# Kernel optimization log

Measured on AMD Instinct MI355X. Metric: run time of the kernel, lower is better.

## Reference

```python
import jax, jax.numpy as jnp
from jax import lax
import numpy as np

EPS = 1e-5
N_BITS = 2   # sign-random-projection hash bits
U = 0.999    # ALSH filter rescale constant (from module args)


def _conv(x, w, b):
    # 3x3, stride 1, pad 1, NCHW/OIHW
    y = lax.conv_general_dilated(x, w, (1, 1), ((1, 1), (1, 1)),
                                 dimension_numbers=('NCHW', 'OIHW', 'NCHW'))
    return y + b[None, :, None, None]


def _bn2d(x, g, b):
    m = x.mean((0, 2, 3), keepdims=True)
    v = x.var((0, 2, 3), keepdims=True)
    return (x - m) * lax.rsqrt(v + EPS) * g[None, :, None, None] + b[None, :, None, None]


def _bn1d(x, g, b):
    m = x.mean(0)
    v = x.var(0)
    return (x - m) * lax.rsqrt(v + EPS) * g + b


def _pool(x):
    return lax.reduce_window(x, -jnp.inf, lax.max, (1, 1, 2, 2), (1, 1, 2, 2), 'VALID')


def _alsh_mask(x, w6, hash_a):
    # ALSH-MIPS filter selection with SignRandomProjection.
    C_out = w6.shape[0]
    wf = w6.reshape(C_out, -1)                       # (256, 2304)
    norms = jnp.linalg.norm(wf, axis=1)
    wf_s = wf * (U / jnp.max(norms))                 # rescale so max norm = U
    ns = jnp.linalg.norm(wf_s, axis=1)
    # P = append_sub_norm_powers (m=2): [w, ||w||^2, ||w||^4]
    P = jnp.concatenate([wf_s, (ns ** 2)[:, None], (ns ** 4)[:, None]], axis=1)
    # Query: mean input patch (per-channel mean tiled over 3x3 taps), normalized
    q = x.mean((0, 2, 3))                            # (256,)
    qv = jnp.tile(q, 9)
    qv = qv / (jnp.linalg.norm(qv) + 1e-12)
    Q = jnp.concatenate([qv, jnp.zeros((2,), x.dtype)])  # append_zeros (m=2)
    bits_f = (P @ hash_a.T) > 0                      # (256, N_BITS)
    bits_q = (Q @ hash_a.T) > 0                      # (N_BITS,)
    pw = 2 ** jnp.arange(N_BITS)
    code_f = (bits_f * pw).sum(1)
    code_q = (bits_q * pw).sum()
    return lax.stop_gradient((code_f == code_q).astype(x.dtype))  # (256,)


def setup_inputs() -> dict:
    key = jax.random.key(0)
    ks = jax.random.split(key, 12)
    B = 256
    d = {}
    d['x'] = jax.random.normal(ks[0], (B, 3, 32, 32), jnp.float32)
    conv_shapes = [(64, 3), (64, 64), (128, 64), (128, 128), (256, 128), (256, 256)]
    for i, (co, ci) in enumerate(conv_shapes, start=1):
        d[f'w{i}'] = jax.random.normal(ks[i], (co, ci, 3, 3), jnp.float32) * 0.05
        d[f'b{i}'] = jnp.zeros((co,), jnp.float32)
        d[f'g{i}'] = jnp.ones((co,), jnp.float32)
        d[f'be{i}'] = jnp.zeros((co,), jnp.float32)
    d['hash_a'] = jax.random.normal(ks[7], (N_BITS, 256 * 9 + 2), jnp.float32)
    d['fc7_w'] = jax.random.normal(ks[8], (512, 4096), jnp.float32) * 0.02
    d['fc7_b'] = jnp.zeros((512,), jnp.float32)
    d['g7'] = jnp.ones((512,), jnp.float32)
    d['be7'] = jnp.zeros((512,), jnp.float32)
    d['fc8_w'] = jax.random.normal(ks[9], (512, 512), jnp.float32) * 0.02
    d['fc8_b'] = jnp.zeros((512,), jnp.float32)
    d['g8'] = jnp.ones((512,), jnp.float32)
    d['be8'] = jnp.zeros((512,), jnp.float32)
    d['fc9_w'] = jax.random.normal(ks[10], (10, 512), jnp.float32) * 0.02
    d['fc9_b'] = jnp.zeros((10,), jnp.float32)
    return d


def reference(x, w1, b1, g1, be1, w2, b2, g2, be2, w3, b3, g3, be3,
              w4, b4, g4, be4, w5, b5, g5, be5, w6, b6, g6, be6, hash_a,
              fc7_w, fc7_b, g7, be7, fc8_w, fc8_b, g8, be8, fc9_w, fc9_b):
    B = x.shape[0]
    x = jax.nn.relu(_bn2d(_conv(x, w1, b1), g1, be1))
    x = jax.nn.relu(_bn2d(_conv(x, w2, b2), g2, be2))
    x = _pool(x)                                   # (B,64,16,16)
    x = jax.nn.relu(_bn2d(_conv(x, w3, b3), g3, be3))
    x = jax.nn.relu(_bn2d(_conv(x, w4, b4), g4, be4))
    x = _pool(x)                                   # (B,128,8,8)
    x = jax.nn.relu(_bn2d(_conv(x, w5, b5), g5, be5))  # (B,256,8,8)
    # ALSH conv6: compute only hash-matched filters, zero-fill the rest.
    mask = _alsh_mask(x, w6, hash_a)               # (256,)
    x = _conv(x, w6, b6) * mask[None, :, None, None]   # subset conv + zero_fill_missing
    x = jax.nn.relu(_bn2d(x, g6, be6))
    x = _pool(x)                                   # (B,256,4,4)
    x = x.reshape(B, -1)                           # (B,4096)
    x = jax.nn.relu(_bn1d(x @ fc7_w.T + fc7_b, g7, be7))
    x = jax.nn.relu(_bn1d(x @ fc8_w.T + fc8_b, g8, be8))
    return x @ fc9_w.T + fc9_b                     # (B,10)
```

## Files before the change

### kernel.cpp

```cpp
#include <hip/hip_runtime.h>

typedef unsigned short u16;
typedef unsigned int u32;
typedef __attribute__((ext_vector_type(8))) _Float16 f16x8;
typedef __attribute__((ext_vector_type(4))) float f32x4;

#define U_CONST 0.999f

constexpr size_t OFFB_STATS = 0;
constexpr size_t OFFB_WSTAT = 14336;
constexpr size_t OFFB_MASK  = 18432;
constexpr size_t OFFB_FCIN  = 32768;
constexpr size_t OFFB_W7T   = 2129920;
constexpr size_t OFFB_W8T   = 6324224;
constexpr size_t OFFB_P7    = 6848512;
constexpr size_t OFFB_P8    = 15237120;
constexpr size_t OFFB_A7    = 19431424;
constexpr size_t OFFB_A8    = 19693568;
constexpr size_t OFFB_WT2   = 20971520;
constexpr size_t OFFB_WT3   = 21045248;
constexpr size_t OFFB_WT4   = 21192704;
constexpr size_t OFFB_WT5   = 21487616;
constexpr size_t OFFB_WT6   = 22077440;
constexpr size_t OFFB_SLAB1 = 25165824;
constexpr size_t OFFB_SLAB2 = 60817408;
constexpr size_t OFFB_PART  = OFFB_P7;
constexpr size_t OFFB_QPART = OFFB_P8;

__device__ __forceinline__ u16 f2h(float f) {
  _Float16 h = (_Float16)f;
  return __builtin_bit_cast(u16, h);
}
__device__ __forceinline__ float h2f(u16 u) {
  return (float)__builtin_bit_cast(_Float16, u);
}
__device__ __forceinline__ void gload16(const void* g, void* l) {
  __builtin_amdgcn_global_load_lds(
      (const __attribute__((address_space(1))) unsigned int*)g,
      (__attribute__((address_space(3))) unsigned int*)l, 16, 0, 0);
}

__global__ __launch_bounds__(256) void k_xform_x(const float* __restrict__ x,
                                                 float* __restrict__ xt) {
  int idx = blockIdx.x * 256 + threadIdx.x;
  if (idx >= 256 * 3 * 1024) return;
  int c = idx % 3;
  int t = idx / 3;
  int s = t % 1024;
  int b = t / 1024;
  xt[idx] = x[(b * 3 + c) * 1024 + s];
}

__global__ __launch_bounds__(256) void k_xform_w(const float* __restrict__ w,
                                                 u16* __restrict__ wt, int CO,
                                                 int CI) {
  int total = CO * CI * 9;
  for (int idx = blockIdx.x * 256 + threadIdx.x; idx < total;
       idx += gridDim.x * 256) {
    int ci = idx % CI;
    int t = idx / CI;
    int co = t % CO;
    int tap = t / CO;
    wt[idx] = f2h(w[(co * CI + ci) * 9 + tap]);
  }
}

__global__ __launch_bounds__(256) void k_cvt_h(const float* __restrict__ w,
                                               u16* __restrict__ o, int n) {
  for (int i = blockIdx.x * 256 + threadIdx.x; i < n; i += gridDim.x * 256)
    o[i] = f2h(w[i]);
}

__global__ __launch_bounds__(256) void k_conv1(const float* __restrict__ xt,
                                               const float* __restrict__ w1,
                                               const float* __restrict__ b1,
                                               u16* __restrict__ y,
                                               float* __restrict__ part) {
  __shared__ float Ins[4 * 34 * 3];
  __shared__ float Ws[27 * 64];
  __shared__ float sred[64 * 16 * 2];
  int tid = threadIdx.x;
  int m0 = blockIdx.x * 64;
  int b = m0 >> 10;
  int y0 = (m0 & 1023) >> 5;

  for (int i = tid; i < 27 * 64; i += 256) {
    int co = i & 63;
    int t = i >> 6;
    int ci = t % 3;
    int tap = t / 3;
    Ws[i] = w1[co * 27 + ci * 9 + tap];
  }
  for (int i = tid; i < 4 * 34 * 3; i += 256) {
    int ci = i % 3;
    int t = i / 3;
    int xx = t % 34;
    int yy = t / 34;
    int gy = y0 - 1 + yy;
    int gx = xx - 1;
    float v = 0.f;
    if ((unsigned)gy < 32u && (unsigned)gx < 32u)
      v = xt[((b * 32 + gy) * 32 + gx) * 3 + ci];
    Ins[i] = v;
  }
  __syncthreads();

  int tr = tid >> 4, tc = tid & 15;
  float acc[4][4] = {};
#pragma unroll
  for (int tap = 0; tap < 9; tap++) {
    int dy = tap / 3, dx = tap % 3;
#pragma unroll
    for (int ci = 0; ci < 3; ci++) {
      float4 wv = *(const float4*)&Ws[(tap * 3 + ci) * 64 + tc * 4];
#pragma unroll
      for (int i = 0; i < 4; i++) {
        int r = tr * 4 + i;
        int yy = (r >> 5) + dy;
        int xx = (r & 31) + dx;
        float a = Ins[(yy * 34 + xx) * 3 + ci];
        acc[i][0] += a * wv.x;
        acc[i][1] += a * wv.y;
        acc[i][2] += a * wv.z;
        acc[i][3] += a * wv.w;
      }
    }
  }
  float4 bb = *(const float4*)&b1[tc * 4];
  float cs[4] = {}, cq[4] = {};
#pragma unroll
  for (int i = 0; i < 4; i++) {
    size_t r = (size_t)(m0 + tr * 4 + i);
    float v0 = acc[i][0] + bb.x, v1 = acc[i][1] + bb.y;
    float v2 = acc[i][2] + bb.z, v3 = acc[i][3] + bb.w;
    cs[0] += v0; cq[0] += v0 * v0;
    cs[1] += v1; cq[1] += v1 * v1;
    cs[2] += v2; cq[2] += v2 * v2;
    cs[3] += v3; cq[3] += v3 * v3;
    u32 lo = (u32)f2h(v0) | ((u32)f2h(v1) << 16);
    u32 hi = (u32)f2h(v2) | ((u32)f2h(v3) << 16);
    *(uint2*)&y[r * 64 + tc * 4] = make_uint2(lo, hi);
  }
#pragma unroll
  for (int q = 0; q < 4; q++) {
    sred[((tc * 4 + q) * 16 + tr) * 2] = cs[q];
    sred[((tc * 4 + q) * 16 + tr) * 2 + 1] = cq[q];
  }
  __syncthreads();
  if (tid < 64) {
    float s = 0.f, q = 0.f;
#pragma unroll
    for (int t = 0; t < 16; t++) {
      s += sred[(tid * 16 + t) * 2];
      q += sred[(tid * 16 + t) * 2 + 1];
    }
    part[(size_t)tid * gridDim.x + blockIdx.x] = s;
    part[(size_t)(64 + tid) * gridDim.x + blockIdx.x] = q;
  }
}

template <int CIN, int COUT, int H, int W, bool MASKED>
__global__ __launch_bounds__(256) void k_cmfma(
    const u16* __restrict__ inp, const u16* __restrict__ wt,
    const float* __restrict__ bias, const float* __restrict__ mask,
    u16* __restrict__ out, float* __restrict__ part) {
  constexpr int HW = H * W;
  __shared__ __align__(16) u16 ldsA[128 * 64];
  __shared__ __align__(16) u16 ldsB[64 * 64];
  const int tid = threadIdx.x;
  const int wave = tid >> 6, lane = tid & 63;
  const int m0 = blockIdx.x * 128;
  const int n0 = blockIdx.y * 64;
  const int ss = (lane & 7) ^ (lane >> 3);
  const u16* aptr[4];
#pragma unroll
  for (int q = 0; q < 4; q++) {
    int m = m0 + wave * 32 + q * 8 + (lane >> 3);
    int b = m / HW, rem = m % HW;
    int yy = rem / W, xx = rem % W;
    aptr[q] = inp +
              ((size_t)((b * (H + 2) + yy + 1) * (W + 2)) + xx + 1) * CIN +
              ss * 8;
  }
  const u16* bptr[2];
#pragma unroll
  for (int q = 0; q < 2; q++) {
    int rb = wave * 16 + q * 8 + (lane >> 3);
    bptr[q] = wt + (size_t)(n0 + rb) * CIN + ss * 8;
  }
  u16* lA = ldsA + wave * 32 * 64;
  u16* lB = ldsB + wave * 16 * 64;
  const int arow0 = wave * 32 + (lane & 15);
  const int nrow = lane & 15;
  const int t0 = lane >> 4, x7 = lane & 7;
  f32x4 acc[2][4] = {};

#pragma unroll 1
  for (int tap = 0; tap < 9; tap++) {
    const int aoff = (tap / 3 - 1) * ((W + 2) * CIN) + (tap % 3 - 1) * CIN;
    const size_t woff = (size_t)tap * COUT * CIN;
#pragma unroll 1
    for (int c0 = 0; c0 < CIN; c0 += 64) {
      __syncthreads();
#pragma unroll
      for (int q = 0; q < 4; q++) gload16(aptr[q] + aoff + c0, lA + q * 512);
#pragma unroll
      for (int q = 0; q < 2; q++) gload16(bptr[q] + woff + c0, lB + q * 512);
      __syncthreads();
#pragma unroll
      for (int h = 0; h < 2; h++) {
        const int sl = (((h << 2) + t0) ^ x7) * 8;
        f16x8 af[2], bf[4];
#pragma unroll
        for (int i = 0; i < 2; i++)
          af[i] = *(const f16x8*)&ldsA[(arow0 + i * 16) * 64 + sl];
#pragma unroll
        for (int j = 0; j < 4; j++)
          bf[j] = *(const f16x8*)&ldsB[(nrow + j * 16) * 64 + sl];
#pragma unroll
        for (int i = 0; i < 2; i++)
#pragma unroll
          for (int j = 0; j < 4; j++)
            acc[i][j] = __builtin_amdgcn_mfma_f32_16x16x32_f16(
                af[i], bf[j], acc[i][j], 0, 0, 0);
      }
    }
  }
  float bn[4], mk[4];
#pragma unroll
  for (int j = 0; j < 4; j++) {
    int n = n0 + j * 16 + nrow;
    bn[j] = bias[n];
    mk[j] = MASKED ? mask[n] : 1.f;
  }
  float ps[4] = {}, pq[4] = {};
#pragma unroll
  for (int i = 0; i < 2; i++)
#pragma unroll
    for (int r = 0; r < 4; r++) {
      int m = m0 + wave * 32 + i * 16 + (lane >> 4) * 4 + r;
#pragma unroll
      for (int j = 0; j < 4; j++) {
        float v = acc[i][j][r] + bn[j];
        if (MASKED) v *= mk[j];
        out[(size_t)m * COUT + n0 + j * 16 + nrow] = f2h(v);
        ps[j] += v;
        pq[j] += v * v;
      }
    }
#pragma unroll
  for (int j = 0; j < 4; j++) {
    ps[j] += __shfl_xor(ps[j], 16);
    pq[j] += __shfl_xor(pq[j], 16);
    ps[j] += __shfl_xor(ps[j], 32);
    pq[j] += __shfl_xor(pq[j], 32);
  }
  __syncthreads();
  float* red = (float*)ldsA;
  if (lane < 16) {
#pragma unroll
    for (int j = 0; j < 4; j++) {
      red[(wave * 64 + j * 16 + lane) * 2] = ps[j];
      red[(wave * 64 + j * 16 + lane) * 2 + 1] = pq[j];
    }
  }
  __syncthreads();
  if (tid < 64) {
    float s = 0.f, q = 0.f;
#pragma unroll
    for (int w = 0; w < 4; w++) {
      s += red[(w * 64 + tid) * 2];
      q += red[(w * 64 + tid) * 2 + 1];
    }
    part[(size_t)(n0 + tid) * gridDim.x + blockIdx.x] = s;
    part[(size_t)(COUT + n0 + tid) * gridDim.x + blockIdx.x] = q;
  }
}

__global__ __launch_bounds__(256) void k_redstat(const float* __restrict__ part,
                                                 float* __restrict__ stats,
                                                 int NB, int C) {
  int c = blockIdx.x;
  const float* ps = part + (size_t)c * NB;
  const float* pq = part + (size_t)(C + c) * NB;
  int tid = threadIdx.x;
  float s = 0.f, q = 0.f;
  for (int t = tid; t < NB; t += 256) {
    s += ps[t];
    q += pq[t];
  }
#pragma unroll
  for (int off = 32; off > 0; off >>= 1) {
    s += __shfl_xor(s, off);
    q += __shfl_xor(q, off);
  }
  __shared__ float r2[4][2];
  int wave = tid >> 6, lane = tid & 63;
  if (lane == 0) {
    r2[wave][0] = s;
    r2[wave][1] = q;
  }
  __syncthreads();
  if (tid == 0) {
    stats[c * 2] = r2[0][0] + r2[1][0] + r2[2][0] + r2[3][0];
    stats[c * 2 + 1] = r2[0][1] + r2[1][1] + r2[2][1] + r2[3][1];
  }
}

__global__ __launch_bounds__(256) void k_qred(const float* __restrict__ qpart,
                                              float* __restrict__ qstat,
                                              int NB) {
  int c = blockIdx.x;
  const float* ps = qpart + (size_t)c * NB;
  int tid = threadIdx.x;
  float s = 0.f;
  for (int t = tid; t < NB; t += 256) s += ps[t];
#pragma unroll
  for (int off = 32; off > 0; off >>= 1) s += __shfl_xor(s, off);
  __shared__ float r2[4];
  int wave = tid >> 6, lane = tid & 63;
  if (lane == 0) r2[wave] = s;
  __syncthreads();
  if (tid == 0) qstat[c] = r2[0] + r2[1] + r2[2] + r2[3];
}

template <int C, int H, int W, bool QSUM>
__global__ __launch_bounds__(256) void k_bnrelu_pad(
    const u16* __restrict__ y, float invN, const float* __restrict__ st,
    const float* __restrict__ g, const float* __restrict__ be,
    u16* __restrict__ outp, float* __restrict__ qpart) {
  constexpr int CH8 = C / 8, HP = H + 2, WP = W + 2;
  __shared__ float sA[C], sB[C];
  __shared__ float qred[QSUM ? 4 : 1][32][8];
  int tid = threadIdx.x;
  if (tid < C) {
    float mu = st[tid * 2] * invN;
    float var = st[tid * 2 + 1] * invN - mu * mu;
    float sc = g[tid] * rsqrtf(var + 1e-5f);
    sA[tid] = sc;
    sB[tid] = be[tid] - mu * sc;
  }
  __syncthreads();
  float qs[8] = {};
  const size_t T = (size_t)256 * HP * WP * CH8;
  for (size_t i = (size_t)blockIdx.x * 256 + tid; i < T;
       i += (size_t)gridDim.x * 256) {
    int slot = (int)(i % CH8);
    size_t t = i / CH8;
    int xx = (int)(t % WP);
    t /= WP;
    int yy = (int)(t % HP);
    int b = (int)(t / HP);
    uint4 o;
    if (yy == 0 || yy == HP - 1 || xx == 0 || xx == WP - 1) {
      o = make_uint4(0u, 0u, 0u, 0u);
    } else {
      uint4 v =
          ((const uint4*)y)[(((size_t)(b * H + yy - 1) * W) + xx - 1) * CH8 +
                            slot];
      u32 pv[4] = {v.x, v.y, v.z, v.w};
      u32 po[4];
      int c0 = slot * 8;
#pragma unroll
      for (int k = 0; k < 4; k++) {
        int c = c0 + 2 * k;
        float lo = fmaxf(h2f((u16)(pv[k] & 0xffffu)) * sA[c] + sB[c], 0.f);
        float hi =
            fmaxf(h2f((u16)(pv[k] >> 16)) * sA[c + 1] + sB[c + 1], 0.f);
        if (QSUM) {
          qs[2 * k] += lo;
          qs[2 * k + 1] += hi;
        }
        po[k] = (u32)f2h(lo) | ((u32)f2h(hi) << 16);
      }
      o = make_uint4(po[0], po[1], po[2], po[3]);
    }
    ((uint4*)outp)[i] = o;
  }
  if (QSUM) {
    int wave = tid >> 6, lane = tid & 63;
#pragma unroll
    for (int j = 0; j < 8; j++) qs[j] += __shfl_xor(qs[j], 32);
    if (lane < 32) {
#pragma unroll
      for (int j = 0; j < 8; j++) qred[wave][lane][j] = qs[j];
    }
    __syncthreads();
    int slot = tid >> 3, jj = tid & 7;
    float s = qred[0][slot][jj] + qred[1][slot][jj] + qred[2][slot][jj] +
              qred[3][slot][jj];
    qpart[(size_t)(slot * 8 + jj) * gridDim.x + blockIdx.x] = s;
  }
}

template <int C, int H, int W, bool NCHW>
__global__ __launch_bounds__(256) void k_bnpool(
    const u16* __restrict__ y, float invN, const float* __restrict__ st,
    const float* __restrict__ g, const float* __restrict__ be,
    void* __restrict__ outv) {
  constexpr int CH8 = C / 8, HO = H / 2, WO = W / 2;
  constexpr int HP = NCHW ? HO : HO + 2, WP = NCHW ? WO : WO + 2;
  __shared__ float sA[C], sB[C];
  int tid = threadIdx.x;
  if (tid < C) {
    float mu = st[tid * 2] * invN;
    float var = st[tid * 2 + 1] * invN - mu * mu;
    float sc = g[tid] * rsqrtf(var + 1e-5f);
    sA[tid] = sc;
    sB[tid] = be[tid] - mu * sc;
  }
  __syncthreads();
  const size_t T = (size_t)256 * HP * WP * CH8;
  for (size_t i = (size_t)blockIdx.x * 256 + tid; i < T;
       i += (size_t)gridDim.x * 256) {
    int slot = (int)(i % CH8);
    size_t t = i / CH8;
    int xx = (int)(t % WP);
    t /= WP;
    int yy = (int)(t % HP);
    int b = (int)(t / HP);
    int px, py;
    bool border = false;
    if (NCHW) {
      px = xx;
      py = yy;
    } else {
      px = xx - 1;
      py = yy - 1;
      border = (yy == 0 || yy == HP - 1 || xx == 0 || xx == WP - 1);
    }
    if (border) {
      ((uint4*)outv)[i] = make_uint4(0u, 0u, 0u, 0u);
      continue;
    }
    const uint4* yp = (const uint4*)y;
    size_t i00 = (((size_t)(b * H + 2 * py) * W) + 2 * px) * CH8 + slot;
    uint4 v00 = yp[i00], v01 = yp[i00 + CH8];
    uint4 v10 = yp[i00 + (size_t)W * CH8], v11 = yp[i00 + (size_t)W * CH8 + CH8];
    u32 p00[4] = {v00.x, v00.y, v00.z, v00.w};
    u32 p01[4] = {v01.x, v01.y, v01.z, v01.w};
    u32 p10[4] = {v10.x, v10.y, v10.z, v10.w};
    u32 p11[4] = {v11.x, v11.y, v11.z, v11.w};
    int c0 = slot * 8;
    float r[8];
#pragma unroll
    for (int k = 0; k < 4; k++) {
      int c = c0 + 2 * k;
      float a_ = sA[c], b_ = sB[c], a2 = sA[c + 1], b2 = sB[c + 1];
      float l0 = fmaxf(h2f((u16)(p00[k] & 0xffffu)) * a_ + b_, 0.f);
      float l1 = fmaxf(h2f((u16)(p01[k] & 0xffffu)) * a_ + b_, 0.f);
      float l2 = fmaxf(h2f((u16)(p10[k] & 0xffffu)) * a_ + b_, 0.f);
      float l3 = fmaxf(h2f((u16)(p11[k] & 0xffffu)) * a_ + b_, 0.f);
      float h0 = fmaxf(h2f((u16)(p00[k] >> 16)) * a2 + b2, 0.f);
      float h1 = fmaxf(h2f((u16)(p01[k] >> 16)) * a2 + b2, 0.f);
      float h2 = fmaxf(h2f((u16)(p10[k] >> 16)) * a2 + b2, 0.f);
      float h3 = fmaxf(h2f((u16)(p11[k] >> 16)) * a2 + b2, 0.f);
      r[2 * k] = fmaxf(fmaxf(l0, l1), fmaxf(l2, l3));
      r[2 * k + 1] = fmaxf(fmaxf(h0, h1), fmaxf(h2, h3));
    }
    if (NCHW) {
      u16* of = (u16*)outv;
#pragma unroll
      for (int j = 0; j < 8; j++)
        of[((size_t)(b * C + c0 + j) * HO + py) * WO + px] = f2h(r[j]);
    } else {
      u32 po[4];
#pragma unroll
      for (int k = 0; k < 4; k++)
        po[k] = (u32)f2h(r[2 * k]) | ((u32)f2h(r[2 * k + 1]) << 16);
      ((uint4*)outv)[i] = make_uint4(po[0], po[1], po[2], po[3]);
    }
  }
}

template <int K, int KSPLIT>
__global__ __launch_bounds__(256) void k_fcmfma(const u16* __restrict__ a,
                                                const u16* __restrict__ w,
                                                float* __restrict__ p) {
  constexpr int KCH = K / KSPLIT;
  __shared__ __align__(16) u16 ldsA[128 * 64];
  __shared__ __align__(16) u16 ldsB[64 * 64];
  const int tid = threadIdx.x;
  const int wave = tid >> 6, lane = tid & 63;
  const int m0 = blockIdx.x * 128;
  const int n0 = blockIdx.y * 64;
  const int ks = blockIdx.z;
  const int ss = (lane & 7) ^ (lane >> 3);
  const u16* aptr[4];
#pragma unroll
  for (int q = 0; q < 4; q++)
    aptr[q] = a + (size_t)(m0 + wave * 32 + q * 8 + (lane >> 3)) * K + ss * 8;
  const u16* bptr[2];
#pragma unroll
  for (int q = 0; q < 2; q++)
    bptr[q] = w + (size_t)(n0 + wave * 16 + q * 8 + (lane >> 3)) * K + ss * 8;
  u16* lA = ldsA + wave * 32 * 64;
  u16* lB = ldsB + wave * 16 * 64;
  const int arow0 = wave * 32 + (lane & 15);
  const int nrow = lane & 15;
  const int t0 = lane >> 4, x7 = lane & 7;
  f32x4 acc[2][4] = {};

#pragma unroll 1
  for (int kc = ks * KCH; kc < ks * KCH + KCH; kc += 64) {
    __syncthreads();
#pragma unroll
    for (int q = 0; q < 4; q++) gload16(aptr[q] + kc, lA + q * 512);
#pragma unroll
    for (int q = 0; q < 2; q++) gload16(bptr[q] + kc, lB + q * 512);
    __syncthreads();
#pragma unroll
    for (int h = 0; h < 2; h++) {
      const int sl = (((h << 2) + t0) ^ x7) * 8;
      f16x8 af[2], bf[4];
#pragma unroll
      for (int i = 0; i < 2; i++)
        af[i] = *(const f16x8*)&ldsA[(arow0 + i * 16) * 64 + sl];
#pragma unroll
      for (int j = 0; j < 4; j++)
        bf[j] = *(const f16x8*)&ldsB[(nrow + j * 16) * 64 + sl];
#pragma unroll
      for (int i = 0; i < 2; i++)
#pragma unroll
        for (int j = 0; j < 4; j++)
          acc[i][j] = __builtin_amdgcn_mfma_f32_16x16x32_f16(
              af[i], bf[j], acc[i][j], 0, 0, 0);
    }
  }
  float* po = p + (size_t)ks * (256 * 512);
#pragma unroll
  for (int i = 0; i < 2; i++)
#pragma unroll
    for (int r = 0; r < 4; r++) {
      int m = m0 + wave * 32 + i * 16 + (lane >> 4) * 4 + r;
#pragma unroll
      for (int j = 0; j < 4; j++)
        po[(size_t)m * 512 + n0 + j * 16 + nrow] = acc[i][j][r];
    }
}

template <int NS>
__global__ __launch_bounds__(256) void k_bn1dfuse(const float* __restrict__ p,
                                                  const float* __restrict__ g,
                                                  const float* __restrict__ be,
                                                  u16* __restrict__ outp) {
  int wave = threadIdx.x >> 6, lane = threadIdx.x & 63;
  int c = blockIdx.x * 4 + wave;
  float v[4] = {};
#pragma unroll 1
  for (int s = 0; s < NS; s++) {
    const float* ps = p + (size_t)s * (256 * 512);
#pragma unroll
    for (int r = 0; r < 4; r++) v[r] += ps[(size_t)(lane + r * 64) * 512 + c];
  }
  float s1 = v[0] + v[1] + v[2] + v[3];
  float s2 = v[0] * v[0] + v[1] * v[1] + v[2] * v[2] + v[3] * v[3];
#pragma unroll
  for (int off = 32; off > 0; off >>= 1) {
    s1 += __shfl_xor(s1, off);
    s2 += __shfl_xor(s2, off);
  }
  float mu = s1 * (1.f / 256.f);
  float var = s2 * (1.f / 256.f) - mu * mu;
  float sc = g[c] * rsqrtf(var + 1e-5f);
  float sh = be[c] - mu * sc;
#pragma unroll
  for (int r = 0; r < 4; r++) {
    float y = fmaxf(v[r] * sc + sh, 0.f);
    outp[(size_t)(lane + r * 64) * 512 + c] = f2h(y);
  }
}

__global__ __launch_bounds__(256) void k_fc9(const u16* __restrict__ a,
                                             const float* __restrict__ w,
                                             const float* __restrict__ bias,
                                             float* __restrict__ out) {
  int b = blockIdx.x, tid = threadIdx.x;
  int o = tid & 15, ch = tid >> 4;
  float s = 0.f;
  if (o < 10) {
    const u16* ap = a + (size_t)b * 512 + ch * 32;
    const float* wp = w + (size_t)o * 512 + ch * 32;
#pragma unroll
    for (int k = 0; k < 32; k++) s += h2f(ap[k]) * wp[k];
  }
  __shared__ float red[16][17];
  red[ch][o] = s;
  __syncthreads();
  if (tid < 10) {
    float t = bias[tid];
#pragma unroll
    for (int c2 = 0; c2 < 16; c2++) t += red[c2][tid];
    out[b * 10 + tid] = t;
  }
}

__global__ __launch_bounds__(256) void k_w6stats(const float* __restrict__ w6,
                                                 const float* __restrict__ ha,
                                                 float* __restrict__ wstats) {
  int f = blockIdx.x, tid = threadIdx.x;
  const float* wp = w6 + (size_t)f * 2304;
  float ss = 0.f, d0 = 0.f, d1 = 0.f;
#pragma unroll
  for (int k = 0; k < 9; k++) {
    float v = wp[k * 256 + tid];
    ss += v * v;
    d0 += v * ha[k * 256 + tid];
    d1 += v * ha[2306 + k * 256 + tid];
  }
  for (int off = 32; off > 0; off >>= 1) {
    ss += __shfl_down(ss, off);
    d0 += __shfl_down(d0, off);
    d1 += __shfl_down(d1, off);
  }
  __shared__ float r[4][3];
  int wv = tid >> 6, ln = tid & 63;
  if (ln == 0) {
    r[wv][0] = ss;
    r[wv][1] = d0;
    r[wv][2] = d1;
  }
  __syncthreads();
  if (tid == 0) {
    float a0 = 0.f, a1 = 0.f, a2 = 0.f;
    for (int i = 0; i < 4; i++) {
      a0 += r[i][0];
      a1 += r[i][1];
      a2 += r[i][2];
    }
    wstats[f * 4 + 0] = a0;
    wstats[f * 4 + 1] = a1;
    wstats[f * 4 + 2] = a2;
  }
}

__global__ __launch_bounds__(256) void k_mask(const float* __restrict__ wstats,
                                              const float* __restrict__ qstats,
                                              const float* __restrict__ ha,
                                              float invN,
                                              float* __restrict__ mask) {
  int tid = threadIdx.x;
  __shared__ float red[256];
  float n2 = wstats[tid * 4];
  red[tid] = n2;
  __syncthreads();
  for (int off = 128; off > 0; off >>= 1) {
    if (tid < off) red[tid] = fmaxf(red[tid], red[tid + off]);
    __syncthreads();
  }
  float maxn2 = red[0];
  float qm = qstats[tid] * invN;
  float h0 = 0.f, h1 = 0.f;
#pragma unroll
  for (int k = 0; k < 9; k++) {
    h0 += ha[k * 256 + tid];
    h1 += ha[2306 + k * 256 + tid];
  }
  __shared__ float r0[256], r1[256];
  r0[tid] = qm * h0;
  r1[tid] = qm * h1;
  __syncthreads();
  for (int off = 128; off > 0; off >>= 1) {
    if (tid < off) {
      r0[tid] += r0[tid + off];
      r1[tid] += r1[tid + off];
    }
    __syncthreads();
  }
  float qd0 = r0[0], qd1 = r1[0];
  float s = U_CONST / sqrtf(maxn2);
  float ns2 = s * s * wstats[tid * 4];
  float v0 = s * wstats[tid * 4 + 1] + ns2 * ha[2304] + ns2 * ns2 * ha[2305];
  float v1 = s * wstats[tid * 4 + 2] + ns2 * ha[2306 + 2304] +
             ns2 * ns2 * ha[2306 + 2305];
  bool bf0 = v0 > 0.f, bf1 = v1 > 0.f;
  bool bq0 = qd0 > 0.f, bq1 = qd1 > 0.f;
  mask[tid] = (bf0 == bq0 && bf1 == bq1) ? 1.f : 0.f;
}

extern "C" void kernel_launch(void* const* d_in, const int* in_sizes, int n_in,
                              void* d_out, int out_size, void* d_ws,
                              size_t ws_size, hipStream_t stream) {
  (void)in_sizes; (void)n_in; (void)out_size; (void)ws_size;
  const float* x = (const float*)d_in[0];
  const float* w1 = (const float*)d_in[1];
  const float* b1 = (const float*)d_in[2];
  const float* g1 = (const float*)d_in[3];
  const float* be1 = (const float*)d_in[4];
  const float* w2 = (const float*)d_in[5];
  const float* b2 = (const float*)d_in[6];
  const float* g2 = (const float*)d_in[7];
  const float* be2 = (const float*)d_in[8];
  const float* w3 = (const float*)d_in[9];
  const float* b3 = (const float*)d_in[10];
  const float* g3 = (const float*)d_in[11];
  const float* be3 = (const float*)d_in[12];
  const float* w4 = (const float*)d_in[13];
  const float* b4 = (const float*)d_in[14];
  const float* g4 = (const float*)d_in[15];
  const float* be4 = (const float*)d_in[16];
  const float* w5 = (const float*)d_in[17];
  const float* b5 = (const float*)d_in[18];
  const float* g5 = (const float*)d_in[19];
  const float* be5 = (const float*)d_in[20];
  const float* w6 = (const float*)d_in[21];
  const float* b6 = (const float*)d_in[22];
  const float* g6 = (const float*)d_in[23];
  const float* be6 = (const float*)d_in[24];
  const float* hash_a = (const float*)d_in[25];
  const float* fc7_w = (const float*)d_in[26];
  const float* g7 = (const float*)d_in[28];
  const float* be7 = (const float*)d_in[29];
  const float* fc8_w = (const float*)d_in[30];
  const float* g8 = (const float*)d_in[32];
  const float* be8 = (const float*)d_in[33];
  const float* fc9_w = (const float*)d_in[34];
  const float* fc9_b = (const float*)d_in[35];

  char* wsb = (char*)d_ws;
  float* stats = (float*)(wsb + OFFB_STATS);
  float* wstats = (float*)(wsb + OFFB_WSTAT);
  float* maskb = (float*)(wsb + OFFB_MASK);
  u16* fcin = (u16*)(wsb + OFFB_FCIN);
  u16* w7t = (u16*)(wsb + OFFB_W7T);
  u16* w8t = (u16*)(wsb + OFFB_W8T);
  float* p7 = (float*)(wsb + OFFB_P7);
  float* p8 = (float*)(wsb + OFFB_P8);
  u16* a7 = (u16*)(wsb + OFFB_A7);
  u16* a8 = (u16*)(wsb + OFFB_A8);
  float* part = (float*)(wsb + OFFB_PART);
  float* qpart = (float*)(wsb + OFFB_QPART);
  u16* wt2 = (u16*)(wsb + OFFB_WT2);
  u16* wt3 = (u16*)(wsb + OFFB_WT3);
  u16* wt4 = (u16*)(wsb + OFFB_WT4);
  u16* wt5 = (u16*)(wsb + OFFB_WT5);
  u16* wt6 = (u16*)(wsb + OFFB_WT6);
  u16* slab1 = (u16*)(wsb + OFFB_SLAB1);
  u16* slab2 = (u16*)(wsb + OFFB_SLAB2);
  float* xt = (float*)(wsb + OFFB_SLAB2);
  float* outp = (float*)d_out;

  k_xform_x<<<3072, 256, 0, stream>>>(x, xt);
  k_xform_w<<<144, 256, 0, stream>>>(w2, wt2, 64, 64);
  k_xform_w<<<288, 256, 0, stream>>>(w3, wt3, 128, 64);
  k_xform_w<<<576, 256, 0, stream>>>(w4, wt4, 128, 128);
  k_xform_w<<<1152, 256, 0, stream>>>(w5, wt5, 256, 128);
  k_xform_w<<<2304, 256, 0, stream>>>(w6, wt6, 256, 256);
  k_cvt_h<<<2048, 256, 0, stream>>>(fc7_w, w7t, 512 * 4096);
  k_cvt_h<<<256, 256, 0, stream>>>(fc8_w, w8t, 512 * 512);
  k_w6stats<<<256, 256, 0, stream>>>(w6, hash_a, wstats);

  k_conv1<<<4096, 256, 0, stream>>>(xt, w1, b1, slab1, part);
  k_redstat<<<64, 256, 0, stream>>>(part, stats + 0, 4096, 64);
  k_bnrelu_pad<64, 32, 32, false><<<1024, 256, 0, stream>>>(
      slab1, 1.f / 262144.f, stats + 0, g1, be1, slab2, nullptr);
  k_cmfma<64, 64, 32, 32, false><<<dim3(2048, 1), 256, 0, stream>>>(
      slab2, wt2, b2, nullptr, slab1, part);
  k_redstat<<<64, 256, 0, stream>>>(part, stats + 512, 2048, 64);
  k_bnpool<64, 32, 32, false><<<512, 256, 0, stream>>>(
      slab1, 1.f / 262144.f, stats + 512, g2, be2, slab2);
  k_cmfma<64, 128, 16, 16, false><<<dim3(512, 2), 256, 0, stream>>>(
      slab2, wt3, b3, nullptr, slab1, part);
  k_redstat<<<128, 256, 0, stream>>>(part, stats + 1024, 512, 128);
  k_bnrelu_pad<128, 16, 16, false><<<1024, 256, 0, stream>>>(
      slab1, 1.f / 65536.f, stats + 1024, g3, be3, slab2, nullptr);
  k_cmfma<128, 128, 16, 16, false><<<dim3(512, 2), 256, 0, stream>>>(
      slab2, wt4, b4, nullptr, slab1, part);
  k_redstat<<<128, 256, 0, stream>>>(part, stats + 1536, 512, 128);
  k_bnpool<128, 16, 16, false><<<512, 256, 0, stream>>>(
      slab1, 1.f / 65536.f, stats + 1536, g4, be4, slab2);
  k_cmfma<128, 256, 8, 8, false><<<dim3(128, 4), 256, 0, stream>>>(
      slab2, wt5, b5, nullptr, slab1, part);
  k_redstat<<<256, 256, 0, stream>>>(part, stats + 2048, 128, 256);
  k_bnrelu_pad<256, 8, 8, true><<<1024, 256, 0, stream>>>(
      slab1, 1.f / 16384.f, stats + 2048, g5, be5, slab2, qpart);
  k_qred<<<256, 256, 0, stream>>>(qpart, stats + 3072, 1024);
  k_mask<<<1, 256, 0, stream>>>(wstats, stats + 3072, hash_a, 1.f / 16384.f,
                                maskb);
  k_cmfma<256, 256, 8, 8, true><<<dim3(128, 4), 256, 0, stream>>>(
      slab2, wt6, b6, maskb, slab1, part);
  k_redstat<<<256, 256, 0, stream>>>(part, stats + 2560, 128, 256);
  k_bnpool<256, 8, 8, true><<<512, 256, 0, stream>>>(
      slab1, 1.f / 16384.f, stats + 2560, g6, be6, fcin);
  k_fcmfma<4096, 16><<<dim3(2, 8, 16), 256, 0, stream>>>(fcin, w7t, p7);
  k_bn1dfuse<16><<<128, 256, 0, stream>>>(p7, g7, be7, a7);
  k_fcmfma<512, 8><<<dim3(2, 8, 8), 256, 0, stream>>>(a7, w8t, p8);
  k_bn1dfuse<8><<<128, 256, 0, stream>>>(p8, g8, be8, a8);
  k_fc9<<<256, 256, 0, stream>>>(a8, fc9_w, fc9_b, outp);
}
```

Before: 427.3 us.

## Enlarge conv MFMA tiles, fuse weight-prep kernels, read NCHW input directly in conv1

The conv MFMA kernel is templated on a per-block wave grid (WM x WN). Each wave now computes a 64x64 output tile with a 4x4 accumulator array instead of 32x64, so blocks cover 256x64 or 128x128 and launch half as many. This raises per-wave MFMA work per LDS load and reuses staged A and B tiles more. All weight-transform and fp16-conversion launches merge into one kernel, and conv1 reads NCHW input directly, which drops the input transpose kernel. The cost is more accumulator registers per thread, possibly lower occupancy, and fewer blocks on the smaller layers.

```diff
diff --git a/kernel.cpp b/kernel.cpp
--- a/kernel.cpp
+++ b/kernel.cpp
@@ -40,43 +40,45 @@
       (__attribute__((address_space(3))) unsigned int*)l, 16, 0, 0);
 }
 
-__global__ __launch_bounds__(256) void k_xform_x(const float* __restrict__ x,
-                                                 float* __restrict__ xt) {
-  int idx = blockIdx.x * 256 + threadIdx.x;
-  if (idx >= 256 * 3 * 1024) return;
-  int c = idx % 3;
-  int t = idx / 3;
-  int s = t % 1024;
-  int b = t / 1024;
-  xt[idx] = x[(b * 3 + c) * 1024 + s];
-}
-
-__global__ __launch_bounds__(256) void k_xform_w(const float* __restrict__ w,
-                                                 u16* __restrict__ wt, int CO,
-                                                 int CI) {
-  int total = CO * CI * 9;
-  for (int idx = blockIdx.x * 256 + threadIdx.x; idx < total;
-       idx += gridDim.x * 256) {
-    int ci = idx % CI;
-    int t = idx / CI;
-    int co = t % CO;
-    int tap = t / CO;
-    wt[idx] = f2h(w[(co * CI + ci) * 9 + tap]);
-  }
-}
-
-__global__ __launch_bounds__(256) void k_cvt_h(const float* __restrict__ w,
-                                               u16* __restrict__ o, int n) {
-  for (int i = blockIdx.x * 256 + threadIdx.x; i < n; i += gridDim.x * 256)
-    o[i] = f2h(w[i]);
-}
-
-__global__ __launch_bounds__(256) void k_conv1(const float* __restrict__ xt,
+__global__ __launch_bounds__(256) void k_wprep(
+    const float* __restrict__ w2, const float* __restrict__ w3,
+    const float* __restrict__ w4, const float* __restrict__ w5,
+    const float* __restrict__ w6, const float* __restrict__ f7,
+    const float* __restrict__ f8, u16* __restrict__ o2, u16* __restrict__ o3,
+    u16* __restrict__ o4, u16* __restrict__ o5, u16* __restrict__ o6,
+    u16* __restrict__ o7, u16* __restrict__ o8) {
+  for (int i = blockIdx.x * 256 + threadIdx.x; i < 3502080;
+       i += gridDim.x * 256) {
+    if (i < 1142784) {
+      const float* w;
+      u16* o;
+      int e, CO, CI;
+      if (i < 36864) { w = w2; o = o2; e = i; CO = 64; CI = 64; }
+      else if (i < 110592) { w = w3; o = o3; e = i - 36864; CO = 128; CI = 64; }
+      else if (i < 258048) { w = w4; o = o4; e = i - 110592; CO = 128; CI = 128; }
+      else if (i < 552960) { w = w5; o = o5; e = i - 258048; CO = 256; CI = 128; }
+      else { w = w6; o = o6; e = i - 552960; CO = 256; CI = 256; }
+      int ci = e % CI;
+      int t = e / CI;
+      int co = t % CO;
+      int tap = t / CO;
+      o[e] = f2h(w[(co * CI + ci) * 9 + tap]);
+    } else if (i < 3239936) {
+      int e = i - 1142784;
+      o7[e] = f2h(f7[e]);
+    } else {
+      int e = i - 3239936;
+      o8[e] = f2h(f8[e]);
+    }
+  }
+}
+
+__global__ __launch_bounds__(256) void k_conv1(const float* __restrict__ x,
                                                const float* __restrict__ w1,
                                                const float* __restrict__ b1,
                                                u16* __restrict__ y,
                                                float* __restrict__ part) {
-  __shared__ float Ins[4 * 34 * 3];
+  __shared__ float Ins[3 * 4 * 34];
   __shared__ float Ws[27 * 64];
   __shared__ float sred[64 * 16 * 2];
   int tid = threadIdx.x;
@@ -91,16 +93,16 @@
     int tap = t / 3;
     Ws[i] = w1[co * 27 + ci * 9 + tap];
   }
-  for (int i = tid; i < 4 * 34 * 3; i += 256) {
-    int ci = i % 3;
-    int t = i / 3;
-    int xx = t % 34;
-    int yy = t / 34;
+  for (int i = tid; i < 3 * 4 * 34; i += 256) {
+    int xx = i % 34;
+    int t = i / 34;
+    int yy = t & 3;
+    int ci = t >> 2;
     int gy = y0 - 1 + yy;
     int gx = xx - 1;
     float v = 0.f;
     if ((unsigned)gy < 32u && (unsigned)gx < 32u)
-      v = xt[((b * 32 + gy) * 32 + gx) * 3 + ci];
+      v = x[((size_t)(b * 3 + ci) * 32 + gy) * 32 + gx];
     Ins[i] = v;
   }
   __syncthreads();
@@ -118,7 +120,7 @@
         int r = tr * 4 + i;
         int yy = (r >> 5) + dy;
         int xx = (r & 31) + dx;
-        float a = Ins[(yy * 34 + xx) * 3 + ci];
+        float a = Ins[(ci * 4 + yy) * 34 + xx];
         acc[i][0] += a * wv.x;
         acc[i][1] += a * wv.y;
         acc[i][2] += a * wv.z;
@@ -159,41 +161,46 @@
   }
 }
 
-template <int CIN, int COUT, int H, int W, bool MASKED>
+template <int CIN, int COUT, int H, int W, int WM, int WN, bool MASKED>
 __global__ __launch_bounds__(256) void k_cmfma(
     const u16* __restrict__ inp, const u16* __restrict__ wt,
     const float* __restrict__ bias, const float* __restrict__ mask,
     u16* __restrict__ out, float* __restrict__ part) {
   constexpr int HW = H * W;
-  __shared__ __align__(16) u16 ldsA[128 * 64];
-  __shared__ __align__(16) u16 ldsB[64 * 64];
+  constexpr int BM = WM * 64, BN = WN * 64;
+  constexpr int RPW = BM / 4;
+  constexpr int RBW = BN / 4;
+  constexpr int ALD = RPW / 8;
+  constexpr int BLD = RBW / 8;
+  __shared__ __align__(16) u16 ldsA[BM * 64];
+  __shared__ __align__(16) u16 ldsB[BN * 64];
   const int tid = threadIdx.x;
   const int wave = tid >> 6, lane = tid & 63;
-  const int m0 = blockIdx.x * 128;
-  const int n0 = blockIdx.y * 64;
+  const int m0 = blockIdx.x * BM;
+  const int n0 = blockIdx.y * BN;
   const int ss = (lane & 7) ^ (lane >> 3);
-  const u16* aptr[4];
-#pragma unroll
-  for (int q = 0; q < 4; q++) {
-    int m = m0 + wave * 32 + q * 8 + (lane >> 3);
+  const u16* aptr[ALD];
+#pragma unroll
+  for (int q = 0; q < ALD; q++) {
+    int m = m0 + wave * RPW + q * 8 + (lane >> 3);
     int b = m / HW, rem = m % HW;
     int yy = rem / W, xx = rem % W;
     aptr[q] = inp +
               ((size_t)((b * (H + 2) + yy + 1) * (W + 2)) + xx + 1) * CIN +
               ss * 8;
   }
-  const u16* bptr[2];
-#pragma unroll
-  for (int q = 0; q < 2; q++) {
-    int rb = wave * 16 + q * 8 + (lane >> 3);
-    bptr[q] = wt + (size_t)(n0 + rb) * CIN + ss * 8;
-  }
-  u16* lA = ldsA + wave * 32 * 64;
-  u16* lB = ldsB + wave * 16 * 64;
-  const int arow0 = wave * 32 + (lane & 15);
-  const int nrow = lane & 15;
+  const u16* bptr[BLD];
+#pragma unroll
+  for (int q = 0; q < BLD; q++) {
+    int rb = n0 + wave * RBW + q * 8 + (lane >> 3);
+    bptr[q] = wt + (size_t)rb * CIN + ss * 8;
+  }
+  u16* lA = ldsA + wave * RPW * 64;
+  u16* lB = ldsB + wave * RBW * 64;
+  const int wm = wave / WN, wn = wave % WN;
+  const int fr = lane & 15;
   const int t0 = lane >> 4, x7 = lane & 7;
-  f32x4 acc[2][4] = {};
+  f32x4 acc[4][4] = {};
 
 #pragma unroll 1
   for (int tap = 0; tap < 9; tap++) {
@@ -203,22 +210,22 @@
     for (int c0 = 0; c0 < CIN; c0 += 64) {
       __syncthreads();
 #pragma unroll
-      for (int q = 0; q < 4; q++) gload16(aptr[q] + aoff + c0, lA + q * 512);
-#pragma unroll
-      for (int q = 0; q < 2; q++) gload16(bptr[q] + woff + c0, lB + q * 512);
+      for (int q = 0; q < ALD; q++) gload16(aptr[q] + aoff + c0, lA + q * 512);
+#pragma unroll
+      for (int q = 0; q < BLD; q++) gload16(bptr[q] + woff + c0, lB + q * 512);
       __syncthreads();
 #pragma unroll
       for (int h = 0; h < 2; h++) {
         const int sl = (((h << 2) + t0) ^ x7) * 8;
-        f16x8 af[2], bf[4];
-#pragma unroll
-        for (int i = 0; i < 2; i++)
-          af[i] = *(const f16x8*)&ldsA[(arow0 + i * 16) * 64 + sl];
+        f16x8 af[4], bf[4];
+#pragma unroll
+        for (int i = 0; i < 4; i++)
+          af[i] = *(const f16x8*)&ldsA[(wm * 64 + i * 16 + fr) * 64 + sl];
 #pragma unroll
         for (int j = 0; j < 4; j++)
-          bf[j] = *(const f16x8*)&ldsB[(nrow + j * 16) * 64 + sl];
-#pragma unroll
-        for (int i = 0; i < 2; i++)
+          bf[j] = *(const f16x8*)&ldsB[(wn * 64 + j * 16 + fr) * 64 + sl];
+#pragma unroll
+        for (int i = 0; i < 4; i++)
 #pragma unroll
           for (int j = 0; j < 4; j++)
             acc[i][j] = __builtin_amdgcn_mfma_f32_16x16x32_f16(
@@ -229,21 +236,21 @@
   float bn[4], mk[4];
 #pragma unroll
   for (int j = 0; j < 4; j++) {
-    int n = n0 + j * 16 + nrow;
+    int n = n0 + wn * 64 + j * 16 + fr;
     bn[j] = bias[n];
     mk[j] = MASKED ? mask[n] : 1.f;
   }
   float ps[4] = {}, pq[4] = {};
 #pragma unroll
-  for (int i = 0; i < 2; i++)
+  for (int i = 0; i < 4; i++)
 #pragma unroll
     for (int r = 0; r < 4; r++) {
-      int m = m0 + wave * 32 + i * 16 + (lane >> 4) * 4 + r;
+      int m = m0 + wm * 64 + i * 16 + t0 * 4 + r;
 #pragma unroll
       for (int j = 0; j < 4; j++) {
         float v = acc[i][j][r] + bn[j];
         if (MASKED) v *= mk[j];
-        out[(size_t)m * COUT + n0 + j * 16 + nrow] = f2h(v);
+        out[(size_t)m * COUT + n0 + wn * 64 + j * 16 + fr] = f2h(v);
         ps[j] += v;
         pq[j] += v * v;
       }
@@ -265,12 +272,13 @@
     }
   }
   __syncthreads();
-  if (tid < 64) {
+  if (tid < 64 * WN) {
+    int wn_t = tid >> 6, cc = tid & 63;
     float s = 0.f, q = 0.f;
 #pragma unroll
-    for (int w = 0; w < 4; w++) {
-      s += red[(w * 64 + tid) * 2];
-      q += red[(w * 64 + tid) * 2 + 1];
+    for (int w = 0; w < WM; w++) {
+      s += red[((w * WN + wn_t) * 64 + cc) * 2];
+      q += red[((w * WN + wn_t) * 64 + cc) * 2 + 1];
     }
     part[(size_t)(n0 + tid) * gridDim.x + blockIdx.x] = s;
     part[(size_t)(COUT + n0 + tid) * gridDim.x + blockIdx.x] = q;
@@ -737,39 +745,32 @@
   u16* wt6 = (u16*)(wsb + OFFB_WT6);
   u16* slab1 = (u16*)(wsb + OFFB_SLAB1);
   u16* slab2 = (u16*)(wsb + OFFB_SLAB2);
-  float* xt = (float*)(wsb + OFFB_SLAB2);
   float* outp = (float*)d_out;
 
-  k_xform_x<<<3072, 256, 0, stream>>>(x, xt);
-  k_xform_w<<<144, 256, 0, stream>>>(w2, wt2, 64, 64);
-  k_xform_w<<<288, 256, 0, stream>>>(w3, wt3, 128, 64);
-  k_xform_w<<<576, 256, 0, stream>>>(w4, wt4, 128, 128);
-  k_xform_w<<<1152, 256, 0, stream>>>(w5, wt5, 256, 128);
-  k_xform_w<<<2304, 256, 0, stream>>>(w6, wt6, 256, 256);
-  k_cvt_h<<<2048, 256, 0, stream>>>(fc7_w, w7t, 512 * 4096);
-  k_cvt_h<<<256, 256, 0, stream>>>(fc8_w, w8t, 512 * 512);
+  k_wprep<<<2048, 256, 0, stream>>>(w2, w3, w4, w5, w6, fc7_w, fc8_w, wt2, wt3,
+                                    wt4, wt5, wt6, w7t, w8t);
   k_w6stats<<<256, 256, 0, stream>>>(w6, hash_a, wstats);
 
-  k_conv1<<<4096, 256, 0, stream>>>(xt, w1, b1, slab1, part);
+  k_conv1<<<4096, 256, 0, stream>>>(x, w1, b1, slab1, part);
   k_redstat<<<64, 256, 0, stream>>>(part, stats + 0, 4096, 64);
   k_bnrelu_pad<64, 32, 32, false><<<1024, 256, 0, stream>>>(
       slab1, 1.f / 262144.f, stats + 0, g1, be1, slab2, nullptr);
-  k_cmfma<64, 64, 32, 32, false><<<dim3(2048, 1), 256, 0, stream>>>(
+  k_cmfma<64, 64, 32, 32, 4, 1, false><<<dim3(1024, 1), 256, 0, stream>>>(
       slab2, wt2, b2, nullptr, slab1, part);
-  k_redstat<<<64, 256, 0, stream>>>(part, stats + 512, 2048, 64);
+  k_redstat<<<64, 256, 0, stream>>>(part, stats + 512, 1024, 64);
   k_bnpool<64, 32, 32, false><<<512, 256, 0, stream>>>(
       slab1, 1.f / 262144.f, stats + 512, g2, be2, slab2);
-  k_cmfma<64, 128, 16, 16, false><<<dim3(512, 2), 256, 0, stream>>>(
+  k_cmfma<64, 128, 16, 16, 2, 2, false><<<dim3(512, 1), 256, 0, stream>>>(
       slab2, wt3, b3, nullptr, slab1, part);
   k_redstat<<<128, 256, 0, stream>>>(part, stats + 1024, 512, 128);
   k_bnrelu_pad<128, 16, 16, false><<<1024, 256, 0, stream>>>(
       slab1, 1.f / 65536.f, stats + 1024, g3, be3, slab2, nullptr);
-  k_cmfma<128, 128, 16, 16, false><<<dim3(512, 2), 256, 0, stream>>>(
+  k_cmfma<128, 128, 16, 16, 2, 2, false><<<dim3(512, 1), 256, 0, stream>>>(
       slab2, wt4, b4, nullptr, slab1, part);
   k_redstat<<<128, 256, 0, stream>>>(part, stats + 1536, 512, 128);
   k_bnpool<128, 16, 16, false><<<512, 256, 0, stream>>>(
       slab1, 1.f / 65536.f, stats + 1536, g4, be4, slab2);
-  k_cmfma<128, 256, 8, 8, false><<<dim3(128, 4), 256, 0, stream>>>(
+  k_cmfma<128, 256, 8, 8, 2, 2, false><<<dim3(128, 2), 256, 0, stream>>>(
       slab2, wt5, b5, nullptr, slab1, part);
   k_redstat<<<256, 256, 0, stream>>>(part, stats + 2048, 128, 256);
   k_bnrelu_pad<256, 8, 8, true><<<1024, 256, 0, stream>>>(
@@ -777,7 +778,7 @@
   k_qred<<<256, 256, 0, stream>>>(qpart, stats + 3072, 1024);
   k_mask<<<1, 256, 0, stream>>>(wstats, stats + 3072, hash_a, 1.f / 16384.f,
                                 maskb);
-  k_cmfma<256, 256, 8, 8, true><<<dim3(128, 4), 256, 0, stream>>>(
+  k_cmfma<256, 256, 8, 8, 2, 2, true><<<dim3(128, 2), 256, 0, stream>>>(
       slab2, wt6, b6, maskb, slab1, part);
   k_redstat<<<256, 256, 0, stream>>>(part, stats + 2560, 128, 256);
   k_bnpool<256, 8, 8, true><<<512, 256, 0, stream>>>(
```

Measured after the change: 424.1 us. Within noise of the previous version (-0.8%).
